# Kernel tuning notes

Measured on AMD Instinct MI355X. Metric: run time of the kernel, lower is better.

## Reference

```python
import jax, jax.numpy as jnp
import numpy as np

B, T = 16384, 128  # batch, n_frames


def setup_inputs() -> dict:
    key = jax.random.key(0)
    k0, k1, k2, k3, k4, k5 = jax.random.split(key, 6)
    dir = jax.random.normal(k0, (B, 3), dtype=jnp.float32)
    R = jax.random.normal(k1, (B, T, 3, 3), dtype=jnp.float32)
    s = 1.0 / np.sqrt(3.0)  # torch LSTM default init scale (uniform +-1/sqrt(hidden))
    W_ih = jax.random.uniform(k2, (12, 3), jnp.float32, -s, s)
    W_hh = jax.random.uniform(k3, (12, 3), jnp.float32, -s, s)
    b_ih = jax.random.uniform(k4, (12,), jnp.float32, -s, s)
    b_hh = jax.random.uniform(k5, (12,), jnp.float32, -s, s)
    return {"dir": dir, "R": R, "W_ih": W_ih, "W_hh": W_hh, "b_ih": b_ih, "b_hh": b_hh}


def _rot_step(v, Rm):
    # v: [B,3], Rm: [B,3,3] -> Rm @ v
    nv = jnp.einsum('bij,bj->bi', Rm, v)
    return nv, nv


def _build_dirs(dir, R):
    n_frames = R.shape[1]
    half = n_frames // 2
    # Backward chain: dirs[i] = R[half-1-i]^T @ ... @ R[half-1]^T @ dir
    Rt_back = jnp.swapaxes(jnp.flip(R[:, :half], axis=1), 2, 3)  # [B, half, 3, 3]
    _, back = jax.lax.scan(_rot_step, dir, jnp.swapaxes(Rt_back, 0, 1))  # [half, B, 3]
    # Forward chain: dirs[i] = R[i-1] @ ... @ R[half] @ dir for i in half+1..n-1
    Rf = jnp.swapaxes(R[:, half:n_frames - 1], 0, 1)  # [n-1-half, B, 3, 3]
    _, fwd = jax.lax.scan(_rot_step, dir, Rf)  # [n-1-half, B, 3]
    dirs_tm = jnp.concatenate([back, dir[None], fwd], axis=0)  # time-major [T, B, 3]
    return dirs_tm, half


def _lstm(dirs_tm, W_ih, W_hh, b_ih, b_hh):
    Bsz = dirs_tm.shape[1]
    h0 = jnp.zeros((Bsz, 3), dirs_tm.dtype)
    c0 = jnp.zeros((Bsz, 3), dirs_tm.dtype)
    bias = b_ih + b_hh

    def step(carry, x):
        h, c = carry
        gates = x @ W_ih.T + h @ W_hh.T + bias  # [B,12]
        i = jax.nn.sigmoid(gates[:, 0:3])
        f = jax.nn.sigmoid(gates[:, 3:6])
        g = jnp.tanh(gates[:, 6:9])
        o = jax.nn.sigmoid(gates[:, 9:12])
        c = f * c + i * g
        h = o * jnp.tanh(c)
        return (h, c), h

    _, h_seq = jax.lax.scan(step, (h0, c0), dirs_tm)  # [T, B, 3]
    return h_seq


def reference(dir, R, W_ih, W_hh, b_ih, b_hh):
    dirs_tm, half = _build_dirs(dir, R)
    h_seq = _lstm(dirs_tm, W_ih, W_hh, b_ih, b_hh)
    dirs_out = jnp.swapaxes(dirs_tm, 0, 1)  # [B, T, 3]
    return dirs_out.at[:, half, :].set(h_seq[half])
```

## Files before the change

kernel.cpp:

```cpp
#include <hip/hip_runtime.h>

typedef float f4 __attribute__((ext_vector_type(4)));
typedef float f4u __attribute__((ext_vector_type(4), aligned(4)));

struct M3 { float m[3][3]; };

#define ELEM(q, n) ((q)[(n) >> 2][(n) & 3])

__device__ __forceinline__ M3 matmul(const M3& A, const M3& B) {
  M3 C;
#pragma unroll
  for (int i = 0; i < 3; ++i)
#pragma unroll
    for (int j = 0; j < 3; ++j)
      C.m[i][j] = A.m[i][0]*B.m[0][j] + A.m[i][1]*B.m[1][j] + A.m[i][2]*B.m[2][j];
  return C;
}

__device__ __forceinline__ M3 mk18(const f4 (&q)[18], int k) {
  M3 A;
#pragma unroll
  for (int i = 0; i < 3; ++i)
#pragma unroll
    for (int j = 0; j < 3; ++j)
      A.m[i][j] = ELEM(q, 9*k + 3*i + j);
  return A;
}

template <int CTRL>
__device__ __forceinline__ float dppf(float v) {
  return __int_as_float(
      __builtin_amdgcn_mov_dpp(__float_as_int(v), CTRL, 0xf, 0xf, true));
}

template <int D>
__device__ __forceinline__ M3 dpp_shr_mat(const M3& A) {
  M3 C;
#pragma unroll
  for (int i = 0; i < 3; ++i)
#pragma unroll
    for (int j = 0; j < 3; ++j)
      C.m[i][j] = dppf<0x110 + D>(A.m[i][j]);
  return C;
}

__device__ __forceinline__ float sigm(float z) {
  return __builtin_amdgcn_rcpf(1.0f + __expf(-z));
}
__device__ __forceinline__ float tanh_(float z) {
  float e = __expf(2.0f * z);
  return 1.0f - 2.0f * __builtin_amdgcn_rcpf(e + 1.0f);
}

template <int CTRL>
__device__ __forceinline__ float quad_bcast(float v) {
  return __int_as_float(
      __builtin_amdgcn_mov_dpp(__float_as_int(v), CTRL, 0xf, 0xf, true));
}

__global__ __launch_bounds__(64, 2) void fused_kernel(
    const float* __restrict__ dir, const float* __restrict__ R,
    const float* __restrict__ Wih, const float* __restrict__ Whh,
    const float* __restrict__ bih, const float* __restrict__ bhh,
    float* __restrict__ out, int B, int nbBack) {
  __shared__ __align__(16) f4 lds[8 * 145];

  const int lane = threadIdx.x;
  const int e = lane >> 3;
  const int s = lane & 7;
  const bool isBack = ((int)blockIdx.x < nbBack);
  const int blk = isBack ? (int)blockIdx.x : ((int)blockIdx.x - nbBack);
  const int b0 = blk * 8;
  const int b = b0 + e;
  const bool valid = (b < B);
  const int bc = valid ? b : (B - 1);
  const int halfOff = isBack ? 0 : 576;

  {
    f4 tb[18];
#pragma unroll
    for (int k = 0; k < 18; ++k) {
      const int c = lane + 64 * k;
      const int ec = c / 144;
      const int rc = c - ec * 144;
      int be = b0 + ec; be = (be < B) ? be : (B - 1);
      tb[k] = *(const f4*)(R + (size_t)be * 1152 + halfOff + rc * 4);
    }
#pragma unroll
    for (int k = 0; k < 18; ++k) {
      const int c = lane + 64 * k;
      const int ec = c / 144;
      const int rc = c - ec * 144;
      lds[ec * 145 + rc] = tb[k];
    }
  }

  f4 q[18];
  {
    const int off = e * 145 + (isBack ? (126 - 18 * s) : (18 * s));
#pragma unroll
    for (int i = 0; i < 18; ++i) q[i] = lds[off + i];
  }

  const float d0 = dir[3*bc+0], d1 = dir[3*bc+1], d2 = dir[3*bc+2];

  M3 P = mk18(q, 0);
#pragma unroll
  for (int k = 1; k < 8; ++k) P = matmul(mk18(q, k), P);

  M3 I = P;
  if (isBack) {
    {
      M3 Sh = dpp_shr_mat<1>(I); M3 T = matmul(Sh, I);
#pragma unroll
      for (int i = 0; i < 3; ++i)
#pragma unroll
        for (int j = 0; j < 3; ++j) I.m[i][j] = (s >= 1) ? T.m[i][j] : I.m[i][j];
    }
    {
      M3 Sh = dpp_shr_mat<2>(I); M3 T = matmul(Sh, I);
#pragma unroll
      for (int i = 0; i < 3; ++i)
#pragma unroll
        for (int j = 0; j < 3; ++j) I.m[i][j] = (s >= 2) ? T.m[i][j] : I.m[i][j];
    }
    {
      M3 Sh = dpp_shr_mat<4>(I); M3 T = matmul(Sh, I);
#pragma unroll
      for (int i = 0; i < 3; ++i)
#pragma unroll
        for (int j = 0; j < 3; ++j) I.m[i][j] = (s >= 4) ? T.m[i][j] : I.m[i][j];
    }
  } else {
    {
      M3 Sh = dpp_shr_mat<1>(I); M3 T = matmul(I, Sh);
#pragma unroll
      for (int i = 0; i < 3; ++i)
#pragma unroll
        for (int j = 0; j < 3; ++j) I.m[i][j] = (s >= 1) ? T.m[i][j] : I.m[i][j];
    }
    {
      M3 Sh = dpp_shr_mat<2>(I); M3 T = matmul(I, Sh);
#pragma unroll
      for (int i = 0; i < 3; ++i)
#pragma unroll
        for (int j = 0; j < 3; ++j) I.m[i][j] = (s >= 2) ? T.m[i][j] : I.m[i][j];
    }
    {
      M3 Sh = dpp_shr_mat<4>(I); M3 T = matmul(I, Sh);
#pragma unroll
      for (int i = 0; i < 3; ++i)
#pragma unroll
        for (int j = 0; j < 3; ++j) I.m[i][j] = (s >= 4) ? T.m[i][j] : I.m[i][j];
    }
  }

  float w0, w1, w2;
  if (isBack) {
    w0 = I.m[0][0]*d0 + I.m[1][0]*d1 + I.m[2][0]*d2;
    w1 = I.m[0][1]*d0 + I.m[1][1]*d1 + I.m[2][1]*d2;
    w2 = I.m[0][2]*d0 + I.m[1][2]*d1 + I.m[2][2]*d2;
  } else {
    w0 = I.m[0][0]*d0 + I.m[0][1]*d1 + I.m[0][2]*d2;
    w1 = I.m[1][0]*d0 + I.m[1][1]*d1 + I.m[1][2]*d2;
    w2 = I.m[2][0]*d0 + I.m[2][1]*d1 + I.m[2][2]*d2;
  }
  float p0 = dppf<0x111>(w0), p1 = dppf<0x111>(w1), p2 = dppf<0x111>(w2);
  float v0 = (s == 0) ? d0 : p0;
  float v1 = (s == 0) ? d1 : p1;
  float v2 = (s == 0) ? d2 : p2;

  float row[24];
  if (isBack) {
#pragma unroll
    for (int j = 0; j < 8; ++j) {
      M3 A = mk18(q, 7 - j);
      float n0 = v0*A.m[0][0] + v1*A.m[1][0] + v2*A.m[2][0];
      float n1 = v0*A.m[0][1] + v1*A.m[1][1] + v2*A.m[2][1];
      float n2 = v0*A.m[0][2] + v1*A.m[1][2] + v2*A.m[2][2];
      v0 = n0; v1 = n1; v2 = n2;
      row[3*j+0] = n0; row[3*j+1] = n1; row[3*j+2] = n2;
    }
  } else {
#pragma unroll
    for (int j = 0; j < 8; ++j) {
      M3 A = mk18(q, j);
      float n0 = A.m[0][0]*v0 + A.m[0][1]*v1 + A.m[0][2]*v2;
      float n1 = A.m[1][0]*v0 + A.m[1][1]*v1 + A.m[1][2]*v2;
      float n2 = A.m[2][0]*v0 + A.m[2][1]*v1 + A.m[2][2]*v2;
      v0 = n0; v1 = n1; v2 = n2;
      row[3*j+0] = n0; row[3*j+1] = n1; row[3*j+2] = n2;
    }
  }

  if (!isBack) {
    if (valid) {
      float* ob = out + (size_t)b * 384 + (size_t)(65 + 8*s) * 3;
#pragma unroll
      for (int kk = 0; kk < 5; ++kk) {
        f4u vv = { row[4*kk+0], row[4*kk+1], row[4*kk+2], row[4*kk+3] };
        *(f4u*)(ob + 4*kk) = vv;
      }
      ob[20] = row[20];
      if (s < 7) { ob[21] = row[21]; ob[22] = row[22]; ob[23] = row[23]; }
    }
    return;
  }

  if (valid) {
    float* ob = out + (size_t)b * 384 + 24 * s;
#pragma unroll
    for (int kk = 0; kk < 6; ++kk) {
      f4 vv = { row[4*kk+0], row[4*kk+1], row[4*kk+2], row[4*kk+3] };
      ((f4*)ob)[kk] = vv;
    }
  }

#pragma unroll
  for (int j = 0; j < 8; ++j) {
    f4 vv = { row[3*j+0], row[3*j+1], row[3*j+2], 0.f };
    lds[(8*s + j) * 9 + e] = vv;
  }

  if (lane >= 32) return;
  const int e2 = lane >> 2;
  const int u = lane & 3, uu = (u == 3) ? 0 : u;
  const int b2 = b0 + e2;
  const bool valid2 = (b2 < B);
  const int b2c = valid2 ? b2 : 0;

  const float wii0 = Wih[uu*3+0],     wii1 = Wih[uu*3+1],     wii2 = Wih[uu*3+2];
  const float wif0 = Wih[(3+uu)*3+0], wif1 = Wih[(3+uu)*3+1], wif2 = Wih[(3+uu)*3+2];
  const float wig0 = Wih[(6+uu)*3+0], wig1 = Wih[(6+uu)*3+1], wig2 = Wih[(6+uu)*3+2];
  const float wio0 = Wih[(9+uu)*3+0], wio1 = Wih[(9+uu)*3+1], wio2 = Wih[(9+uu)*3+2];
  const float whi0 = Whh[uu*3+0],     whi1 = Whh[uu*3+1],     whi2 = Whh[uu*3+2];
  const float whf0 = Whh[(3+uu)*3+0], whf1 = Whh[(3+uu)*3+1], whf2 = Whh[(3+uu)*3+2];
  const float whg0 = Whh[(6+uu)*3+0], whg1 = Whh[(6+uu)*3+1], whg2 = Whh[(6+uu)*3+2];
  const float who0 = Whh[(9+uu)*3+0], who1 = Whh[(9+uu)*3+1], who2 = Whh[(9+uu)*3+2];
  const float bsi = bih[uu]   + bhh[uu];
  const float bsf = bih[3+uu] + bhh[3+uu];
  const float bsg = bih[6+uu] + bhh[6+uu];
  const float bso = bih[9+uu] + bhh[9+uu];
  const float dd0 = dir[3*b2c+0], dd1 = dir[3*b2c+1], dd2 = dir[3*b2c+2];

  float h0 = 0.f, h1 = 0.f, h2 = 0.f, cc = 0.f, hl = 0.f;

#define LSTEP(x0_, x1_, x2_)                                                  \
  {                                                                           \
    float zi = bsi + wii0*(x0_) + wii1*(x1_) + wii2*(x2_)                     \
                   + whi0*h0 + whi1*h1 + whi2*h2;                             \
    float zf = bsf + wif0*(x0_) + wif1*(x1_) + wif2*(x2_)                     \
                   + whf0*h0 + whf1*h1 + whf2*h2;                             \
    float zg = bsg + wig0*(x0_) + wig1*(x1_) + wig2*(x2_)                     \
                   + whg0*h0 + whg1*h1 + whg2*h2;                             \
    float zo = bso + wio0*(x0_) + wio1*(x1_) + wio2*(x2_)                     \
                   + who0*h0 + who1*h1 + who2*h2;                             \
    float ai = sigm(zi), af = sigm(zf), ag = tanh_(zg), ao = sigm(zo);        \
    cc = af*cc + ai*ag;                                                       \
    float hn = ao * tanh_(cc);                                                \
    hl = hn;                                                                  \
    h0 = quad_bcast<0x00>(hn);                                                \
    h1 = quad_bcast<0x55>(hn);                                                \
    h2 = quad_bcast<0xAA>(hn);                                                \
  }

  f4 xa[8], xb[8];
#pragma unroll
  for (int j = 0; j < 8; ++j) xa[j] = lds[j * 9 + e2];
#pragma unroll
  for (int c = 0; c < 8; ++c) {
    if (c < 7) {
      if ((c & 1) == 0) {
#pragma unroll
        for (int j = 0; j < 8; ++j) xb[j] = lds[((c+1)*8 + j) * 9 + e2];
      } else {
#pragma unroll
        for (int j = 0; j < 8; ++j) xa[j] = lds[((c+1)*8 + j) * 9 + e2];
      }
    }
#pragma unroll
    for (int j = 0; j < 8; ++j) {
      f4 x = ((c & 1) == 0) ? xa[j] : xb[j];
      LSTEP(x[0], x[1], x[2]);
    }
  }
  LSTEP(dd0, dd1, dd2);
#undef LSTEP

  if (valid2 && u < 3) out[(size_t)b2 * 384 + 192 + u] = hl;
}

extern "C" void kernel_launch(void* const* d_in, const int* in_sizes, int n_in,
                              void* d_out, int out_size, void* d_ws, size_t ws_size,
                              hipStream_t stream) {
  const float* dir = (const float*)d_in[0];
  const float* R   = (const float*)d_in[1];
  const float* Wih = (const float*)d_in[2];
  const float* Whh = (const float*)d_in[3];
  const float* bih = (const float*)d_in[4];
  const float* bhh = (const float*)d_in[5];
  float* out = (float*)d_out;

  const int B = in_sizes[0] / 3;
  const int nbBack = (B + 7) / 8;
  const int grid = nbBack * 2;
  hipLaunchKernelGGL(fused_kernel, dim3(grid), dim3(64), 0, stream,
                     dir, R, Wih, Whh, bih, bhh, out, B, nbBack);
}
```

Measured before the change: 36.45 us.

## Merge backward and forward chain blocks into one block per batch group

Each block now computes both the backward and the forward rotation chains for its 8 batch elements, which halves the grid. The R matrices are loaded straight from global memory into registers with per-thread strided reads instead of a coalesced stage through LDS. The forward chain's work can now overlap with the LSTM setup in the same wave, and the launch has fewer blocks. In exchange the kernel uses more registers (two 18-vector arrays) and the global loads are less coalesced, which can lower occupancy and memory efficiency.

```diff
diff --git a/kernel.cpp b/kernel.cpp
--- a/kernel.cpp
+++ b/kernel.cpp
@@ -62,54 +62,35 @@
     const float* __restrict__ dir, const float* __restrict__ R,
     const float* __restrict__ Wih, const float* __restrict__ Whh,
     const float* __restrict__ bih, const float* __restrict__ bhh,
-    float* __restrict__ out, int B, int nbBack) {
-  __shared__ __align__(16) f4 lds[8 * 145];
+    float* __restrict__ out, int B) {
+  __shared__ __align__(16) f4 xrows[64 * 9];
 
   const int lane = threadIdx.x;
   const int e = lane >> 3;
   const int s = lane & 7;
-  const bool isBack = ((int)blockIdx.x < nbBack);
-  const int blk = isBack ? (int)blockIdx.x : ((int)blockIdx.x - nbBack);
-  const int b0 = blk * 8;
+  const int b0 = blockIdx.x * 8;
   const int b = b0 + e;
   const bool valid = (b < B);
   const int bc = valid ? b : (B - 1);
-  const int halfOff = isBack ? 0 : 576;
-
+  const f4* Rb4 = (const f4*)(R + (size_t)bc * 1152);
+
+  f4 q[18], qf[18];
   {
-    f4 tb[18];
-#pragma unroll
-    for (int k = 0; k < 18; ++k) {
-      const int c = lane + 64 * k;
-      const int ec = c / 144;
-      const int rc = c - ec * 144;
-      int be = b0 + ec; be = (be < B) ? be : (B - 1);
-      tb[k] = *(const f4*)(R + (size_t)be * 1152 + halfOff + rc * 4);
-    }
-#pragma unroll
-    for (int k = 0; k < 18; ++k) {
-      const int c = lane + 64 * k;
-      const int ec = c / 144;
-      const int rc = c - ec * 144;
-      lds[ec * 145 + rc] = tb[k];
-    }
-  }
-
-  f4 q[18];
+    const f4* pb = Rb4 + 18 * (7 - s);
+    const f4* pf = Rb4 + 144 + 18 * s;
+#pragma unroll
+    for (int i = 0; i < 18; ++i) q[i] = pb[i];
+#pragma unroll
+    for (int i = 0; i < 18; ++i) qf[i] = pf[i];
+  }
+  const float d0 = dir[3*bc+0], d1 = dir[3*bc+1], d2 = dir[3*bc+2];
+
   {
-    const int off = e * 145 + (isBack ? (126 - 18 * s) : (18 * s));
-#pragma unroll
-    for (int i = 0; i < 18; ++i) q[i] = lds[off + i];
-  }
-
-  const float d0 = dir[3*bc+0], d1 = dir[3*bc+1], d2 = dir[3*bc+2];
-
-  M3 P = mk18(q, 0);
-#pragma unroll
-  for (int k = 1; k < 8; ++k) P = matmul(mk18(q, k), P);
-
-  M3 I = P;
-  if (isBack) {
+    M3 P = mk18(q, 0);
+#pragma unroll
+    for (int k = 1; k < 8; ++k) P = matmul(mk18(q, k), P);
+
+    M3 I = P;
     {
       M3 Sh = dpp_shr_mat<1>(I); M3 T = matmul(Sh, I);
 #pragma unroll
@@ -131,47 +112,16 @@
 #pragma unroll
         for (int j = 0; j < 3; ++j) I.m[i][j] = (s >= 4) ? T.m[i][j] : I.m[i][j];
     }
-  } else {
-    {
-      M3 Sh = dpp_shr_mat<1>(I); M3 T = matmul(I, Sh);
-#pragma unroll
-      for (int i = 0; i < 3; ++i)
-#pragma unroll
-        for (int j = 0; j < 3; ++j) I.m[i][j] = (s >= 1) ? T.m[i][j] : I.m[i][j];
-    }
-    {
-      M3 Sh = dpp_shr_mat<2>(I); M3 T = matmul(I, Sh);
-#pragma unroll
-      for (int i = 0; i < 3; ++i)
-#pragma unroll
-        for (int j = 0; j < 3; ++j) I.m[i][j] = (s >= 2) ? T.m[i][j] : I.m[i][j];
-    }
-    {
-      M3 Sh = dpp_shr_mat<4>(I); M3 T = matmul(I, Sh);
-#pragma unroll
-      for (int i = 0; i < 3; ++i)
-#pragma unroll
-        for (int j = 0; j < 3; ++j) I.m[i][j] = (s >= 4) ? T.m[i][j] : I.m[i][j];
-    }
-  }
-
-  float w0, w1, w2;
-  if (isBack) {
-    w0 = I.m[0][0]*d0 + I.m[1][0]*d1 + I.m[2][0]*d2;
-    w1 = I.m[0][1]*d0 + I.m[1][1]*d1 + I.m[2][1]*d2;
-    w2 = I.m[0][2]*d0 + I.m[1][2]*d1 + I.m[2][2]*d2;
-  } else {
-    w0 = I.m[0][0]*d0 + I.m[0][1]*d1 + I.m[0][2]*d2;
-    w1 = I.m[1][0]*d0 + I.m[1][1]*d1 + I.m[1][2]*d2;
-    w2 = I.m[2][0]*d0 + I.m[2][1]*d1 + I.m[2][2]*d2;
-  }
-  float p0 = dppf<0x111>(w0), p1 = dppf<0x111>(w1), p2 = dppf<0x111>(w2);
-  float v0 = (s == 0) ? d0 : p0;
-  float v1 = (s == 0) ? d1 : p1;
-  float v2 = (s == 0) ? d2 : p2;
-
-  float row[24];
-  if (isBack) {
+
+    float w0 = I.m[0][0]*d0 + I.m[1][0]*d1 + I.m[2][0]*d2;
+    float w1 = I.m[0][1]*d0 + I.m[1][1]*d1 + I.m[2][1]*d2;
+    float w2 = I.m[0][2]*d0 + I.m[1][2]*d1 + I.m[2][2]*d2;
+    float p0 = dppf<0x111>(w0), p1 = dppf<0x111>(w1), p2 = dppf<0x111>(w2);
+    float v0 = (s == 0) ? d0 : p0;
+    float v1 = (s == 0) ? d1 : p1;
+    float v2 = (s == 0) ? d2 : p2;
+
+    float row[24];
 #pragma unroll
     for (int j = 0; j < 8; ++j) {
       M3 A = mk18(q, 7 - j);
@@ -181,19 +131,69 @@
       v0 = n0; v1 = n1; v2 = n2;
       row[3*j+0] = n0; row[3*j+1] = n1; row[3*j+2] = n2;
     }
-  } else {
-#pragma unroll
-    for (int j = 0; j < 8; ++j) {
-      M3 A = mk18(q, j);
+
+    if (valid) {
+      float* ob = out + (size_t)b * 384 + 24 * s;
+#pragma unroll
+      for (int kk = 0; kk < 6; ++kk) {
+        f4 vv = { row[4*kk+0], row[4*kk+1], row[4*kk+2], row[4*kk+3] };
+        ((f4*)ob)[kk] = vv;
+      }
+    }
+#pragma unroll
+    for (int j = 0; j < 8; ++j) {
+      f4 vv = { row[3*j+0], row[3*j+1], row[3*j+2], 0.f };
+      xrows[(8*s + j) * 9 + e] = vv;
+    }
+  }
+
+  {
+    M3 P = mk18(qf, 0);
+#pragma unroll
+    for (int k = 1; k < 8; ++k) P = matmul(mk18(qf, k), P);
+
+    M3 I = P;
+    {
+      M3 Sh = dpp_shr_mat<1>(I); M3 T = matmul(I, Sh);
+#pragma unroll
+      for (int i = 0; i < 3; ++i)
+#pragma unroll
+        for (int j = 0; j < 3; ++j) I.m[i][j] = (s >= 1) ? T.m[i][j] : I.m[i][j];
+    }
+    {
+      M3 Sh = dpp_shr_mat<2>(I); M3 T = matmul(I, Sh);
+#pragma unroll
+      for (int i = 0; i < 3; ++i)
+#pragma unroll
+        for (int j = 0; j < 3; ++j) I.m[i][j] = (s >= 2) ? T.m[i][j] : I.m[i][j];
+    }
+    {
+      M3 Sh = dpp_shr_mat<4>(I); M3 T = matmul(I, Sh);
+#pragma unroll
+      for (int i = 0; i < 3; ++i)
+#pragma unroll
+        for (int j = 0; j < 3; ++j) I.m[i][j] = (s >= 4) ? T.m[i][j] : I.m[i][j];
+    }
+
+    float w0 = I.m[0][0]*d0 + I.m[0][1]*d1 + I.m[0][2]*d2;
+    float w1 = I.m[1][0]*d0 + I.m[1][1]*d1 + I.m[1][2]*d2;
+    float w2 = I.m[2][0]*d0 + I.m[2][1]*d1 + I.m[2][2]*d2;
+    float p0 = dppf<0x111>(w0), p1 = dppf<0x111>(w1), p2 = dppf<0x111>(w2);
+    float v0 = (s == 0) ? d0 : p0;
+    float v1 = (s == 0) ? d1 : p1;
+    float v2 = (s == 0) ? d2 : p2;
+
+    float row[24];
+#pragma unroll
+    for (int j = 0; j < 8; ++j) {
+      M3 A = mk18(qf, j);
       float n0 = A.m[0][0]*v0 + A.m[0][1]*v1 + A.m[0][2]*v2;
       float n1 = A.m[1][0]*v0 + A.m[1][1]*v1 + A.m[1][2]*v2;
       float n2 = A.m[2][0]*v0 + A.m[2][1]*v1 + A.m[2][2]*v2;
       v0 = n0; v1 = n1; v2 = n2;
       row[3*j+0] = n0; row[3*j+1] = n1; row[3*j+2] = n2;
     }
-  }
-
-  if (!isBack) {
+
     if (valid) {
       float* ob = out + (size_t)b * 384 + (size_t)(65 + 8*s) * 3;
 #pragma unroll
@@ -204,22 +204,6 @@
       ob[20] = row[20];
       if (s < 7) { ob[21] = row[21]; ob[22] = row[22]; ob[23] = row[23]; }
     }
-    return;
-  }
-
-  if (valid) {
-    float* ob = out + (size_t)b * 384 + 24 * s;
-#pragma unroll
-    for (int kk = 0; kk < 6; ++kk) {
-      f4 vv = { row[4*kk+0], row[4*kk+1], row[4*kk+2], row[4*kk+3] };
-      ((f4*)ob)[kk] = vv;
-    }
-  }
-
-#pragma unroll
-  for (int j = 0; j < 8; ++j) {
-    f4 vv = { row[3*j+0], row[3*j+1], row[3*j+2], 0.f };
-    lds[(8*s + j) * 9 + e] = vv;
   }
 
   if (lane >= 32) return;
@@ -266,16 +250,16 @@
 
   f4 xa[8], xb[8];
 #pragma unroll
-  for (int j = 0; j < 8; ++j) xa[j] = lds[j * 9 + e2];
+  for (int j = 0; j < 8; ++j) xa[j] = xrows[j * 9 + e2];
 #pragma unroll
   for (int c = 0; c < 8; ++c) {
     if (c < 7) {
       if ((c & 1) == 0) {
 #pragma unroll
-        for (int j = 0; j < 8; ++j) xb[j] = lds[((c+1)*8 + j) * 9 + e2];
+        for (int j = 0; j < 8; ++j) xb[j] = xrows[((c+1)*8 + j) * 9 + e2];
       } else {
 #pragma unroll
-        for (int j = 0; j < 8; ++j) xa[j] = lds[((c+1)*8 + j) * 9 + e2];
+        for (int j = 0; j < 8; ++j) xa[j] = xrows[((c+1)*8 + j) * 9 + e2];
       }
     }
 #pragma unroll
@@ -302,8 +286,7 @@
   float* out = (float*)d_out;
 
   const int B = in_sizes[0] / 3;
-  const int nbBack = (B + 7) / 8;
-  const int grid = nbBack * 2;
+  const int grid = (B + 7) / 8;
   hipLaunchKernelGGL(fused_kernel, dim3(grid), dim3(64), 0, stream,
-                     dir, R, Wih, Whh, bih, bhh, out, B, nbBack);
-}
+                     dir, R, Wih, Whh, bih, bhh, out, B);
+}
```

Result: slower. 37.89 us (+3.9%).
